# Kernel tuning notes

Measured on AMD Instinct MI355X. Metric: run time of the kernel, lower is better.

The kernel has to match this reference:

```python
import jax, jax.numpy as jnp
import numpy as np

N = 100000  # nodes (== in_feats, one-hot id features)
E = 3200000  # edges
D = 64       # out_feats == review_feat dim


def setup_inputs() -> dict:
    key = jax.random.key(0)
    k = jax.random.split(key, 7)
    weight = jax.random.normal(k[0], (N, D), dtype=jnp.float32) * 0.05
    ps_w = jax.random.normal(k[1], (1, D), dtype=jnp.float32) * 0.1
    review_feat = jax.random.normal(k[2], (E, D), dtype=jnp.float32)
    cj = jax.random.uniform(k[3], (N, 1), dtype=jnp.float32)
    ci = jax.random.uniform(k[4], (N, 1), dtype=jnp.float32)
    src = jax.random.randint(k[5], (E,), 0, N, dtype=jnp.int32)
    dst = jax.random.randint(k[6], (E,), 0, N, dtype=jnp.int32)
    return {"weight": weight, "ps_w": ps_w, "review_feat": review_feat,
            "cj": cj, "ci": ci, "src": src, "dst": dst}


def reference(weight, ps_w, review_feat, cj, ci, src, dst):
    # feat = dot_or_identity(None, weight) = weight; dropout_rate=0 -> identity
    feat = weight * cj  # [N, D], degree-normalized src features
    # edge gate: sigmoid(Linear(review_feat)) -> [E, 1]
    pa = jax.nn.sigmoid(review_feat @ ps_w.T)  # [E, 1]
    # message = pa * src_h, then segment-sum to dst (fn.sum)
    msg = pa * feat[src]  # [E, D]
    h = jax.ops.segment_sum(msg, dst, num_segments=weight.shape[0])  # [N, D]
    return h * ci
```

## Files before the change

kernel.cpp:

```cpp
#include <hip/hip_runtime.h>


#define SCAN_TILE    2048
#define SCAN_THREADS 512
#define HIST_BLOCKS  256
#define GATE_BLOCKS  2048

__global__ __launch_bounds__(256) void kZW(
    const float* __restrict__ weight,
    const float* __restrict__ cj,
    float*       __restrict__ wcj,
    unsigned*    __restrict__ deg,
    unsigned*    __restrict__ done,
    int N)
{
    const long long tid = (long long)blockIdx.x * 256 + threadIdx.x;
    const long long nthreads = (long long)gridDim.x * 256;
    const long long nq = (long long)N * 16;

    for (long long i = tid; i < nq; i += nthreads) {
        const int n = (int)(i >> 4);
        const float4 w = reinterpret_cast<const float4*>(weight)[i];
        const float c = cj[n];
        reinterpret_cast<float4*>(wcj)[i] = make_float4(w.x * c, w.y * c, w.z * c, w.w * c);
    }
    for (long long i = tid; i < N; i += nthreads) deg[i] = 0u;
    if (tid == 0) *done = 0u;
}

__global__ __launch_bounds__(256) void kM_hist_gate(
    const float* __restrict__ review_feat,
    const float* __restrict__ ps_w,
    const int*   __restrict__ dst,
    float*       __restrict__ scale,
    unsigned*    __restrict__ rank,
    unsigned*    __restrict__ deg,
    int E)
{
    if (blockIdx.x < HIST_BLOCKS) {
        const long long gsz = (long long)HIST_BLOCKS * 256;
        const long long t0  = (long long)blockIdx.x * 256 + threadIdx.x;
        for (long long b = t0; b < E; b += gsz * 4) {
            long long e[4];
            int d[4];
            #pragma unroll
            for (int u = 0; u < 4; ++u) {
                e[u] = b + u * gsz;
                d[u] = (e[u] < E) ? dst[e[u]] : 0;
            }
            unsigned r[4];
            #pragma unroll
            for (int u = 0; u < 4; ++u)
                if (e[u] < E) r[u] = atomicAdd(&deg[d[u]], 1u);
            #pragma unroll
            for (int u = 0; u < 4; ++u)
                if (e[u] < E) rank[e[u]] = r[u];
        }
        return;
    }

    const int bid   = blockIdx.x - HIST_BLOCKS;
    const int lane  = threadIdx.x & 63;
    const int wib   = threadIdx.x >> 6;
    const int group = lane >> 4;
    const int sub   = lane & 15;
    const float4 pw = *reinterpret_cast<const float4*>(ps_w + sub * 4);

    const long long nwaves = (long long)GATE_BLOCKS * 4;
    for (long long w = (long long)bid * 4 + wib; w * 16 < E; w += nwaves) {
        const long long ebase = w * 16;
        float4 rv[4];
        #pragma unroll
        for (int u = 0; u < 4; ++u) {
            const long long e = ebase + u * 4 + group;
            rv[u] = (e < E) ? *reinterpret_cast<const float4*>(review_feat + e * 64 + sub * 4)
                            : make_float4(0.f, 0.f, 0.f, 0.f);
        }
        float x[4];
        #pragma unroll
        for (int u = 0; u < 4; ++u) {
            float t = rv[u].x * pw.x + rv[u].y * pw.y + rv[u].z * pw.z + rv[u].w * pw.w;
            t += __shfl_xor(t, 1);
            t += __shfl_xor(t, 2);
            t += __shfl_xor(t, 4);
            t += __shfl_xor(t, 8);
            x[u] = t;
        }
        if (sub == 0) {
            #pragma unroll
            for (int u = 0; u < 4; ++u) {
                const long long e = ebase + u * 4 + group;
                if (e < E) scale[e] = 1.f / (1.f + __expf(-x[u]));
            }
        }
    }
}

__global__ __launch_bounds__(SCAN_THREADS) void k3_scan_onepass(
    const unsigned* __restrict__ deg,
    unsigned*       __restrict__ offs,
    unsigned*       __restrict__ tileagg,
    unsigned*       __restrict__ done,
    int N, int ntiles)
{
    __shared__ unsigned lds[SCAN_TILE];
    __shared__ unsigned sums[SCAN_THREADS];
    __shared__ unsigned sh_prefix;
    const int t = threadIdx.x;
    const int b = blockIdx.x;
    const int base = b * SCAN_TILE;

    #pragma unroll
    for (int i = 0; i < SCAN_TILE / SCAN_THREADS; ++i) {
        const int idx = base + t + i * SCAN_THREADS;
        lds[t + i * SCAN_THREADS] = (idx < N) ? deg[idx] : 0u;
    }
    __syncthreads();

    unsigned v[SCAN_TILE / SCAN_THREADS];
    unsigned s = 0;
    #pragma unroll
    for (int i = 0; i < SCAN_TILE / SCAN_THREADS; ++i) {
        v[i] = lds[(SCAN_TILE / SCAN_THREADS) * t + i];
        s += v[i];
    }
    sums[t] = s;
    __syncthreads();
    for (int off = 1; off < SCAN_THREADS; off <<= 1) {
        const unsigned x = (t >= off) ? sums[t - off] : 0u;
        __syncthreads();
        sums[t] += x;
        __syncthreads();
    }
    unsigned run = sums[t] - s;
    #pragma unroll
    for (int i = 0; i < SCAN_TILE / SCAN_THREADS; ++i) {
        lds[(SCAN_TILE / SCAN_THREADS) * t + i] = run;
        run += v[i];
    }
    __syncthreads();

    const unsigned agg = sums[SCAN_THREADS - 1];
    if (t == 0) {
        atomicExch(&tileagg[b], agg);
        __threadfence();
        atomicAdd(done, 1u);
        while (atomicAdd(done, 0u) < (unsigned)ntiles) { }
        unsigned p = 0;
        for (int i = 0; i < b; ++i) p += atomicAdd(&tileagg[i], 0u);
        sh_prefix = p;
        if (b == ntiles - 1) offs[N] = p + agg;
    }
    __syncthreads();

    const unsigned pfx = sh_prefix;
    #pragma unroll
    for (int i = 0; i < SCAN_TILE / SCAN_THREADS; ++i) {
        const int idx = base + t + i * SCAN_THREADS;
        if (idx < N) offs[idx] = lds[t + i * SCAN_THREADS] + pfx;
    }
}

__global__ __launch_bounds__(256) void k4_scatter_pure(
    const int*      __restrict__ src,
    const int*      __restrict__ dst,
    const float*    __restrict__ scale,
    const unsigned* __restrict__ rank,
    const unsigned* __restrict__ offs,
    int2*           __restrict__ pairs,
    int E)
{
    const long long gsz = (long long)gridDim.x * blockDim.x;
    const long long t0  = (long long)blockIdx.x * blockDim.x + threadIdx.x;

    long long e[8];
    int s[8], d[8];
    float sc[8];
    unsigned r[8];
    #pragma unroll
    for (int u = 0; u < 8; ++u) {
        e[u] = t0 + u * gsz;
        const bool ok = e[u] < E;
        s[u]  = ok ? src[e[u]]   : 0;
        d[u]  = ok ? dst[e[u]]   : 0;
        sc[u] = ok ? scale[e[u]] : 0.f;
        r[u]  = ok ? rank[e[u]]  : 0u;
    }
    unsigned o[8];
    #pragma unroll
    for (int u = 0; u < 8; ++u)
        o[u] = (e[u] < E) ? offs[d[u]] : 0u;
    #pragma unroll
    for (int u = 0; u < 8; ++u)
        if (e[u] < E) pairs[o[u] + r[u]] = make_int2(s[u], __float_as_int(sc[u]));
}

__global__ __launch_bounds__(256, 4) void k5_gather(
    const float*    __restrict__ wcj,
    const float*    __restrict__ ci,
    const unsigned* __restrict__ offs,
    const int2*     __restrict__ pairs,
    float*          __restrict__ out,
    int N)
{
    const int lane  = threadIdx.x & 63;
    const int wib   = threadIdx.x >> 6;
    const int group = lane >> 4;
    const int sub   = lane & 15;

    const long long n = ((long long)blockIdx.x * 4 + wib) * 4 + group;
    const bool valid = (n < N);

    unsigned start = 0, cnt = 0;
    if (valid) { start = offs[n]; cnt = offs[n + 1] - start; }

    int2 p = make_int2(0, 0);
    if (sub < cnt) p = pairs[start + sub];

    float4 acc = make_float4(0.f, 0.f, 0.f, 0.f);
    for (unsigned k0 = 0; __any((int)(k0 < cnt)); k0 += 16) {
        int2 pn = make_int2(0, 0);
        const unsigned nk = k0 + 16;
        if (nk + sub < cnt) pn = pairs[start + nk + sub];

        int m = (int)cnt - (int)k0;
        if (m > 16) m = 16;
        #pragma unroll 8
        for (int j = 0; j < m; ++j) {
            const int   s  = __shfl(p.x, (group << 4) + j);
            const float sc = __int_as_float(__shfl(p.y, (group << 4) + j));
            const float4 w = *reinterpret_cast<const float4*>(
                wcj + (long long)s * 64 + sub * 4);
            acc.x += sc * w.x;
            acc.y += sc * w.y;
            acc.z += sc * w.z;
            acc.w += sc * w.w;
        }
        p = pn;
    }
    if (valid) {
        const float c = ci[n];
        *reinterpret_cast<float4*>(out + n * 64 + sub * 4) =
            make_float4(acc.x * c, acc.y * c, acc.z * c, acc.w * c);
    }
}

extern "C" void kernel_launch(void* const* d_in, const int* in_sizes, int n_in,
                              void* d_out, int out_size, void* d_ws, size_t ws_size,
                              hipStream_t stream) {
    const float* weight      = (const float*)d_in[0];
    const float* ps_w        = (const float*)d_in[1];
    const float* review_feat = (const float*)d_in[2];
    const float* cj          = (const float*)d_in[3];
    const float* ci          = (const float*)d_in[4];
    const int*   src         = (const int*)d_in[5];
    const int*   dst         = (const int*)d_in[6];
    float*       out         = (float*)d_out;

    const int N = in_sizes[3];
    const int E = in_sizes[5];
    const int ntiles = (N + SCAN_TILE - 1) / SCAN_TILE;

    size_t off = 0;
    auto take = [&](size_t bytes) { size_t o = off; off = (off + bytes + 255) & ~(size_t)255; return o; };
    const size_t pairs_o   = take((size_t)E * 8);
    const size_t scale_o   = take((size_t)E * 4);
    const size_t rank_o    = take((size_t)E * 4);
    const size_t wcj_o     = take((size_t)N * 64 * 4);
    const size_t deg_o     = take((size_t)N * 4);
    const size_t offs_o    = take(((size_t)N + 1) * 4);
    const size_t tileagg_o = take((size_t)ntiles * 4);
    const size_t done_o    = take(4);

    char* base = (char*)d_ws;
    int2*     pairs   = (int2*)    (base + pairs_o);
    float*    scale   = (float*)   (base + scale_o);
    unsigned* rank    = (unsigned*)(base + rank_o);
    float*    wcj     = (float*)   (base + wcj_o);
    unsigned* deg     = (unsigned*)(base + deg_o);
    unsigned* offs    = (unsigned*)(base + offs_o);
    unsigned* tileagg = (unsigned*)(base + tileagg_o);
    unsigned* done    = (unsigned*)(base + done_o);

    kZW<<<1024, 256, 0, stream>>>(weight, cj, wcj, deg, done, N);
    kM_hist_gate<<<HIST_BLOCKS + GATE_BLOCKS, 256, 0, stream>>>(
        review_feat, ps_w, dst, scale, rank, deg, E);
    k3_scan_onepass<<<ntiles, SCAN_THREADS, 0, stream>>>(deg, offs, tileagg, done,
                                                         N, ntiles);
    const int blocks4 = (int)(((long long)E + 8LL * 256 - 1) / (8LL * 256));
    k4_scatter_pure<<<blocks4, 256, 0, stream>>>(src, dst, scale, rank, offs, pairs, E);
    const int blocksD = (N + 15) / 16;
    k5_gather<<<blocksD, 256, 0, stream>>>(wcj, ci, offs, pairs, out, N);
}
```

Baseline: 416.5 us.

## Store prescaled node features in fp16 and fold their computation into scatter kernel

The weight*cj table is now computed inside the scatter kernel, in dedicated extra blocks, and written as fp16 rather than fp32. The first kernel shrinks to zeroing the degree counters. The gather kernel reads half-width rows and converts them to float before accumulating. This halves the bytes of the 3.2M random row gathers and overlaps the table build with the scatter, at the cost of fp16 rounding error in the features.

```diff
diff --git a/kernel.cpp b/kernel.cpp
--- a/kernel.cpp
+++ b/kernel.cpp
@@ -1,31 +1,19 @@
 #include <hip/hip_runtime.h>
+#include <hip/hip_fp16.h>
 
 
 #define SCAN_TILE    2048
 #define SCAN_THREADS 512
 #define HIST_BLOCKS  256
 #define GATE_BLOCKS  2048
-
-__global__ __launch_bounds__(256) void kZW(
-    const float* __restrict__ weight,
-    const float* __restrict__ cj,
-    float*       __restrict__ wcj,
-    unsigned*    __restrict__ deg,
-    unsigned*    __restrict__ done,
-    int N)
-{
-    const long long tid = (long long)blockIdx.x * 256 + threadIdx.x;
-    const long long nthreads = (long long)gridDim.x * 256;
-    const long long nq = (long long)N * 16;
-
-    for (long long i = tid; i < nq; i += nthreads) {
-        const int n = (int)(i >> 4);
-        const float4 w = reinterpret_cast<const float4*>(weight)[i];
-        const float c = cj[n];
-        reinterpret_cast<float4*>(wcj)[i] = make_float4(w.x * c, w.y * c, w.z * c, w.w * c);
-    }
-    for (long long i = tid; i < N; i += nthreads) deg[i] = 0u;
-    if (tid == 0) *done = 0u;
+#define WCJ_BLOCKS   512
+
+__global__ __launch_bounds__(256) void kZ_zero(
+    unsigned* __restrict__ deg, unsigned* __restrict__ done, int n)
+{
+    const int i = blockIdx.x * 256 + threadIdx.x;
+    if (i < n) deg[i] = 0u;
+    if (i == 0) *done = 0u;
 }
 
 __global__ __launch_bounds__(256) void kM_hist_gate(
@@ -161,17 +149,42 @@
     }
 }
 
-__global__ __launch_bounds__(256) void k4_scatter_pure(
+__global__ __launch_bounds__(256) void k4_scatter_wcj(
     const int*      __restrict__ src,
     const int*      __restrict__ dst,
     const float*    __restrict__ scale,
     const unsigned* __restrict__ rank,
     const unsigned* __restrict__ offs,
     int2*           __restrict__ pairs,
-    int E)
-{
-    const long long gsz = (long long)gridDim.x * blockDim.x;
-    const long long t0  = (long long)blockIdx.x * blockDim.x + threadIdx.x;
+    const float*    __restrict__ weight,
+    const float*    __restrict__ cj,
+    __half*         __restrict__ wcj,
+    int E, int N)
+{
+    if (blockIdx.x < WCJ_BLOCKS) {
+        const long long tid = (long long)blockIdx.x * 256 + threadIdx.x;
+        const long long nthreads = (long long)WCJ_BLOCKS * 256;
+        const long long nq = (long long)N * 8;
+        for (long long i = tid; i < nq; i += nthreads) {
+            const int n = (int)(i >> 3);
+            const float4 w0 = reinterpret_cast<const float4*>(weight)[i * 2];
+            const float4 w1 = reinterpret_cast<const float4*>(weight)[i * 2 + 1];
+            const float c = cj[n];
+            const unsigned r0 = (unsigned)__half_as_ushort(__float2half(w0.x * c))
+                              | ((unsigned)__half_as_ushort(__float2half(w0.y * c)) << 16);
+            const unsigned r1 = (unsigned)__half_as_ushort(__float2half(w0.z * c))
+                              | ((unsigned)__half_as_ushort(__float2half(w0.w * c)) << 16);
+            const unsigned r2 = (unsigned)__half_as_ushort(__float2half(w1.x * c))
+                              | ((unsigned)__half_as_ushort(__float2half(w1.y * c)) << 16);
+            const unsigned r3 = (unsigned)__half_as_ushort(__float2half(w1.z * c))
+                              | ((unsigned)__half_as_ushort(__float2half(w1.w * c)) << 16);
+            reinterpret_cast<uint4*>(wcj)[i] = make_uint4(r0, r1, r2, r3);
+        }
+        return;
+    }
+
+    const long long gsz = (long long)(gridDim.x - WCJ_BLOCKS) * 256;
+    const long long t0  = (long long)(blockIdx.x - WCJ_BLOCKS) * 256 + threadIdx.x;
 
     long long e[8];
     int s[8], d[8];
@@ -196,7 +209,7 @@
 }
 
 __global__ __launch_bounds__(256, 4) void k5_gather(
-    const float*    __restrict__ wcj,
+    const __half*   __restrict__ wcj,
     const float*    __restrict__ ci,
     const unsigned* __restrict__ offs,
     const int2*     __restrict__ pairs,
@@ -229,12 +242,12 @@
         for (int j = 0; j < m; ++j) {
             const int   s  = __shfl(p.x, (group << 4) + j);
             const float sc = __int_as_float(__shfl(p.y, (group << 4) + j));
-            const float4 w = *reinterpret_cast<const float4*>(
+            const uint2 raw = *reinterpret_cast<const uint2*>(
                 wcj + (long long)s * 64 + sub * 4);
-            acc.x += sc * w.x;
-            acc.y += sc * w.y;
-            acc.z += sc * w.z;
-            acc.w += sc * w.w;
+            acc.x += sc * __half2float(__ushort_as_half((unsigned short)(raw.x & 0xffffu)));
+            acc.y += sc * __half2float(__ushort_as_half((unsigned short)(raw.x >> 16)));
+            acc.z += sc * __half2float(__ushort_as_half((unsigned short)(raw.y & 0xffffu)));
+            acc.w += sc * __half2float(__ushort_as_half((unsigned short)(raw.y >> 16)));
         }
         p = pn;
     }
@@ -266,7 +279,7 @@
     const size_t pairs_o   = take((size_t)E * 8);
     const size_t scale_o   = take((size_t)E * 4);
     const size_t rank_o    = take((size_t)E * 4);
-    const size_t wcj_o     = take((size_t)N * 64 * 4);
+    const size_t wcj_o     = take((size_t)N * 64 * 2);
     const size_t deg_o     = take((size_t)N * 4);
     const size_t offs_o    = take(((size_t)N + 1) * 4);
     const size_t tileagg_o = take((size_t)ntiles * 4);
@@ -276,19 +289,20 @@
     int2*     pairs   = (int2*)    (base + pairs_o);
     float*    scale   = (float*)   (base + scale_o);
     unsigned* rank    = (unsigned*)(base + rank_o);
-    float*    wcj     = (float*)   (base + wcj_o);
+    __half*   wcj     = (__half*)  (base + wcj_o);
     unsigned* deg     = (unsigned*)(base + deg_o);
     unsigned* offs    = (unsigned*)(base + offs_o);
     unsigned* tileagg = (unsigned*)(base + tileagg_o);
     unsigned* done    = (unsigned*)(base + done_o);
 
-    kZW<<<1024, 256, 0, stream>>>(weight, cj, wcj, deg, done, N);
+    kZ_zero<<<(N + 255) / 256, 256, 0, stream>>>(deg, done, N);
     kM_hist_gate<<<HIST_BLOCKS + GATE_BLOCKS, 256, 0, stream>>>(
         review_feat, ps_w, dst, scale, rank, deg, E);
     k3_scan_onepass<<<ntiles, SCAN_THREADS, 0, stream>>>(deg, offs, tileagg, done,
                                                          N, ntiles);
-    const int blocks4 = (int)(((long long)E + 8LL * 256 - 1) / (8LL * 256));
-    k4_scatter_pure<<<blocks4, 256, 0, stream>>>(src, dst, scale, rank, offs, pairs, E);
+    const int scatterBlocks = (int)(((long long)E + 8LL * 256 - 1) / (8LL * 256));
+    k4_scatter_wcj<<<WCJ_BLOCKS + scatterBlocks, 256, 0, stream>>>(
+        src, dst, scale, rank, offs, pairs, weight, cj, wcj, E, N);
     const int blocksD = (N + 15) / 16;
     k5_gather<<<blocksD, 256, 0, stream>>>(wcj, ci, offs, pairs, out, N);
 }
```

After: 384.5 us. -7.7%, faster.
